# Performance work log

Measured on AMD Instinct MI355X. Metric: run time of the kernel, lower is better.

## Reference

```python
import jax, jax.numpy as jnp
import numpy as np

N = 262144   # tokens
L = 128      # ldims (per-direction LSTM feature size)
H = 128      # hidden_units
H2 = 128     # hidden2_units
R = 64       # number of relation labels


def setup_inputs() -> dict:
    key = jax.random.key(0)
    ks = jax.random.split(key, 12)
    glorot = lambda k, shape: jax.random.uniform(
        k, shape, jnp.float32, -1.0, 1.0) * np.sqrt(6.0 / (shape[0] + shape[1]))
    return {
        "fwd": jax.random.normal(ks[0], (N, L), jnp.float32),
        "bwd": jax.random.normal(ks[1], (N, L), jnp.float32),
        "gold_heads": jax.random.randint(ks[2], (N - 1,), 0, N),
        "gold_rels": jax.random.randint(ks[3], (N - 1,), 0, R),
        "WFOH": glorot(ks[4], (2 * L, H)),
        "WFOM": glorot(ks[5], (2 * L, H)),
        "rhidBias": glorot(ks[6], (1, H)),
        "rcatBias": glorot(ks[7], (1, 2 * H)),
        "rhid2Layer": glorot(ks[8], (2 * H, H2)),
        "rhid2Bias": glorot(ks[9], (1, H2)),
        "routLayer": glorot(ks[10], (H2, R)),
        "routBias": glorot(ks[11], (1, R)),
    }


def reference(fwd, bwd, gold_heads, gold_rels, WFOH, WFOM, rhidBias,
              rcatBias, rhid2Layer, rhid2Bias, routLayer, routBias):
    E = gold_heads.shape[0]
    mods = jnp.arange(E) + 1                       # modifiers are tokens 1..N-1
    # per-edge concat(head fwd-state, modifier bwd-state): (E, 2L)
    cat = jnp.concatenate([fwd[gold_heads], bwd[mods]], axis=-1)
    headfov = cat @ WFOH                           # (E, H)
    modfov = cat @ WFOM                            # (E, H)
    # hidden2_units > 0 branch of __evaluateLabel
    h = jnp.tanh(jnp.concatenate([headfov, modfov], axis=-1) + rcatBias)  # (E, 2H)
    h2 = jnp.tanh(h @ rhid2Layer + rhid2Bias)      # (E, H2)
    scores = h2 @ routLayer + routBias             # (E, R)
    # hinge: best wrong label vs gold label, loss only if margin violated
    gold_s = jnp.take_along_axis(scores, gold_rels[:, None], axis=1)[:, 0]
    masked = jnp.where(jnp.arange(R)[None, :] == gold_rels[:, None], -jnp.inf, scores)
    wrong_idx = jnp.argmax(masked, axis=1)
    wrong_s = jnp.take_along_axis(scores, wrong_idx[:, None], axis=1)[:, 0]
    lerrs = jnp.where(gold_s < wrong_s + 1.0, wrong_s - gold_s, 0.0)  # (E,)
    return lerrs
```

## Files before the change

kernel.cpp:

```cpp
#include <hip/hip_runtime.h>
#include <hip/hip_bf16.h>

typedef __bf16 bf16x8 __attribute__((ext_vector_type(8)));
typedef float  f32x4  __attribute__((ext_vector_type(4)));

#define MFMA16 __builtin_amdgcn_mfma_f32_16x16x32_bf16

__device__ __forceinline__ float fast_tanh(float x) {
    float e = __builtin_amdgcn_exp2f(x * 2.8853900817779268f);
    return 1.0f - 2.0f * __builtin_amdgcn_rcpf(e + 1.0f);
}

__device__ __forceinline__ int kinv(int ke) {
    return (ke & ~31) | ((ke & 1) << 4) | ((ke >> 1) & 15);
}

__device__ __forceinline__ bf16x8 cvt2(const float4 a, const float4 b) {
    bf16x8 t;
    t[0] = (__bf16)a.x; t[1] = (__bf16)a.y; t[2] = (__bf16)a.z; t[3] = (__bf16)a.w;
    t[4] = (__bf16)b.x; t[5] = (__bf16)b.y; t[6] = (__bf16)b.z; t[7] = (__bf16)b.w;
    return t;
}

__global__ __launch_bounds__(256) void preconv_kernel(
    const float* __restrict__ WFOH, const float* __restrict__ WFOM,
    const float* __restrict__ rhid2Layer, const float* __restrict__ routLayer,
    char* __restrict__ ws)
{
    const int f = blockIdx.x * 256 + threadIdx.x;
    bf16x8 v;
    char* dst;
    if (f < 8192) {
        const int lane = f & 63, t = f >> 6;
        const int nbl = t & 1, kk = (t >> 1) & 7, w = t >> 4;
        const int g = lane >> 4, c = lane & 15;
        const int nb = 32 * w + 16 * nbl;
        const float* Wsrc = (nb < 128) ? WFOH : WFOM;
        const int col = (nb + c) & 127;
        #pragma unroll
        for (int j = 0; j < 8; ++j) v[j] = (__bf16)Wsrc[(32 * kk + 8 * g + j) * 128 + col];
        dst = ws + (size_t)f * 16;
    } else if (f < 12288) {
        const int f2 = f - 8192;
        const int lane = f2 & 63, t = f2 >> 6;
        const int nbl = t & 1, kk = (t >> 1) & 7, q4 = t >> 4;
        const int g = lane >> 4, c = lane & 15;
        const int n2 = 32 * q4 + 16 * nbl + c;
        #pragma unroll
        for (int j = 0; j < 8; ++j) v[j] = (__bf16)rhid2Layer[kinv(32 * kk + 8 * g + j) * 128 + n2];
        dst = ws + 131072 + (size_t)f2 * 16;
    } else if (f < 13312) {
        const int f3 = f - 12288;
        const int lane = f3 & 63, t = f3 >> 6;
        const int kk = t & 3, nb = t >> 2;
        const int g = lane >> 4, c = lane & 15;
        const int n3 = 16 * nb + c;
        #pragma unroll
        for (int j = 0; j < 8; ++j) v[j] = (__bf16)routLayer[(32 * kk + 8 * g + j) * 64 + n3];
        dst = ws + 196608 + (size_t)f3 * 16;
    } else {
        return;
    }
    *(bf16x8*)dst = v;
}

template<bool PRE>
__device__ __forceinline__ bf16x8 wfrag1(const char* ws, const float* WFOH, const float* WFOM,
                                         int w, int kk, int nbl, int lane) {
    if constexpr (PRE) {
        return *(const bf16x8*)(ws + (size_t)w * 16384 + kk * 2048 + nbl * 1024 + lane * 16);
    } else {
        const int g = lane >> 4, c = lane & 15;
        const int nb = 32 * w + 16 * nbl;
        const float* Wsrc = (nb < 128) ? WFOH : WFOM;
        const int col = (nb + c) & 127;
        bf16x8 v;
        #pragma unroll
        for (int j = 0; j < 8; ++j) v[j] = (__bf16)Wsrc[(32 * kk + 8 * g + j) * 128 + col];
        return v;
    }
}
template<bool PRE>
__device__ __forceinline__ bf16x8 wfrag2(const char* ws, const float* rhid2Layer,
                                         int q4, int kk, int nbl, int lane) {
    if constexpr (PRE) {
        return *(const bf16x8*)(ws + 131072 + (size_t)q4 * 16384 + kk * 2048 + nbl * 1024 + lane * 16);
    } else {
        const int g = lane >> 4, c = lane & 15;
        const int n2 = 32 * q4 + 16 * nbl + c;
        bf16x8 v;
        #pragma unroll
        for (int j = 0; j < 8; ++j) v[j] = (__bf16)rhid2Layer[kinv(32 * kk + 8 * g + j) * 128 + n2];
        return v;
    }
}
template<bool PRE>
__device__ __forceinline__ bf16x8 wfrag3(const char* ws, const float* routLayer,
                                         int nb, int kk, int lane) {
    if constexpr (PRE) {
        return *(const bf16x8*)(ws + 196608 + (size_t)nb * 4096 + kk * 1024 + lane * 16);
    } else {
        const int g = lane >> 4, c = lane & 15;
        const int n3 = 16 * nb + c;
        bf16x8 v;
        #pragma unroll
        for (int j = 0; j < 8; ++j) v[j] = (__bf16)routLayer[(32 * kk + 8 * g + j) * 64 + n3];
        return v;
    }
}

template<bool PRE>
__global__ __launch_bounds__(512, 2) void rel_kernel(
    const float* __restrict__ fwd, const float* __restrict__ bwd,
    const int* __restrict__ gold_heads, const int* __restrict__ gold_rels,
    const float* __restrict__ WFOH, const float* __restrict__ WFOM,
    const float* __restrict__ rcatBias, const float* __restrict__ rhid2Layer,
    const float* __restrict__ rhid2Bias, const float* __restrict__ routLayer,
    const float* __restrict__ routBias, const char* __restrict__ wstab,
    int* __restrict__ fixcnt, int* __restrict__ fixlist, int fixcap,
    float* __restrict__ out, int E, int NT)
{
    __shared__ __align__(16) char smem[65536];

    const int tid   = threadIdx.x;
    const int w     = tid >> 6;
    const int lane  = tid & 63;
    const int row16 = lane & 15;
    const int g     = lane >> 4;

    const int r_s = tid >> 3;
    const int q_s = tid & 7;

    const float rcb0 = rcatBias[32 * w + row16];
    const float rcb1 = rcatBias[32 * w + 16 + row16];
    const float r2b  = rhid2Bias[16 * w + row16];
    float rob[4];
    #pragma unroll
    for (int nb = 0; nb < 4; ++nb) rob[nb] = routBias[16 * nb + row16];

    bf16x8 pfb[4];
    {
        const int e = blockIdx.x * 64 + r_s;
        int nh0 = 0;
        if (q_s < 4 && e < E) nh0 = gold_heads[e];
        if (e < E) {
            const float* src = (q_s < 4) ? (fwd + (size_t)nh0 * 128 + 32 * q_s)
                                         : (bwd + (size_t)(e + 1) * 128 + 32 * (q_s - 4));
            const float4* p4 = (const float4*)src;
            #pragma unroll
            for (int i = 0; i < 4; ++i) pfb[i] = cvt2(p4[2 * i], p4[2 * i + 1]);
        } else {
            #pragma unroll
            for (int i = 0; i < 4; ++i) pfb[i] = cvt2(make_float4(0.f,0.f,0.f,0.f), make_float4(0.f,0.f,0.f,0.f));
        }
    }

    int pp = 0;
    for (int tile = blockIdx.x; tile < NT; tile += gridDim.x, pp ^= 1) {
        char* const sh_cat = smem + (pp ? 32768 : 0);
        char* const sh_h   = smem + (pp ? 0 : 32768);
        char* const sh_h2  = sh_cat;

        const int e0 = tile * 64;
        const int tnext = tile + gridDim.x;
        const bool hn = tnext < NT;

        int zoff = 0;
        asm volatile("" : "+v"(zoff));
        const char*  wsL  = wstab + zoff;
        const float* W1aL = WFOH + zoff;
        const float* W1bL = WFOM + zoff;
        const float* W2L  = rhid2Layer + zoff;
        const float* W3L  = routLayer + zoff;

        int nh = 0; bool gv = false;
        if (hn) {
            const int en = tnext * 64 + r_s;
            gv = en < E;
            if (q_s < 4 && gv) nh = gold_heads[en];
        }

        #pragma unroll
        for (int i = 0; i < 4; ++i)
            *(bf16x8*)(sh_cat + r_s * 512 + 16 * ((4 * q_s + i + r_s) & 31)) = pfb[i];

        int gr[4] = {0, 0, 0, 0};
        if (w < 4) {
            #pragma unroll
            for (int i = 0; i < 4; ++i) {
                const int e = e0 + 16 * w + 4 * g + i;
                if (e < E) gr[i] = gold_rels[e];
            }
        }
        __syncthreads();

        float4 pfA[8];
        if (hn && gv) {
            const float4* p4 = (const float4*)((q_s < 4)
                                 ? (fwd + (size_t)nh * 128 + 32 * q_s)
                                 : (bwd + (size_t)(tnext * 64 + r_s + 1) * 128 + 32 * (q_s - 4)));
            #pragma unroll
            for (int i = 0; i < 8; ++i) pfA[i] = p4[i];
        } else {
            #pragma unroll
            for (int i = 0; i < 8; ++i) pfA[i] = make_float4(0.f, 0.f, 0.f, 0.f);
        }

        f32x4 acc1[4][2];
        #pragma unroll
        for (int i = 0; i < 4; ++i) {
            acc1[i][0] = (f32x4){0.f, 0.f, 0.f, 0.f};
            acc1[i][1] = (f32x4){0.f, 0.f, 0.f, 0.f};
        }
        __builtin_amdgcn_s_setprio(1);
        #pragma unroll
        for (int kk = 0; kk < 8; ++kk) {
            const bf16x8 b0 = wfrag1<PRE>(wsL, W1aL, W1bL, w, kk, 0, lane);
            const bf16x8 b1 = wfrag1<PRE>(wsL, W1aL, W1bL, w, kk, 1, lane);
            #pragma unroll
            for (int mb = 0; mb < 4; ++mb) {
                const int R = 16 * mb + row16;
                const bf16x8 a = *(const bf16x8*)(sh_cat + R * 512 + 16 * ((4 * kk + g + R) & 31));
                acc1[mb][0] = MFMA16(a, b0, acc1[mb][0], 0, 0, 0);
                acc1[mb][1] = MFMA16(a, b1, acc1[mb][1], 0, 0, 0);
            }
        }
        __builtin_amdgcn_s_setprio(0);
        #pragma unroll
        for (int mb = 0; mb < 4; ++mb) {
            #pragma unroll
            for (int r = 0; r < 4; ++r) {
                const int row = 16 * mb + 4 * g + r;
                const __bf16 p0 = (__bf16)fast_tanh(acc1[mb][0][r] + rcb0);
                const __bf16 p1 = (__bf16)fast_tanh(acc1[mb][1][r] + rcb1);
                const unsigned uval = (unsigned)__builtin_bit_cast(unsigned short, p0)
                                    | ((unsigned)__builtin_bit_cast(unsigned short, p1) << 16);
                const int u = 4 * w + (row16 >> 2);
                *(unsigned*)(sh_h + row * 512 + 16 * ((u + row) & 31) + 4 * (row16 & 3)) = uval;
            }
        }
        __syncthreads();

        f32x4 acc2[4];
        #pragma unroll
        for (int i = 0; i < 4; ++i) acc2[i] = (f32x4){0.f, 0.f, 0.f, 0.f};
        __builtin_amdgcn_s_setprio(1);
        #pragma unroll
        for (int kk = 0; kk < 8; ++kk) {
            const bf16x8 b2 = wfrag2<PRE>(wsL, W2L, w >> 1, kk, w & 1, lane);
            #pragma unroll
            for (int mb = 0; mb < 4; ++mb) {
                const int R = 16 * mb + row16;
                const bf16x8 a = *(const bf16x8*)(sh_h + R * 512 + 16 * ((4 * kk + g + R) & 31));
                acc2[mb] = MFMA16(a, b2, acc2[mb], 0, 0, 0);
            }
        }
        __builtin_amdgcn_s_setprio(0);
        #pragma unroll
        for (int mb = 0; mb < 4; ++mb) {
            #pragma unroll
            for (int r = 0; r < 4; ++r) {
                const int row = 16 * mb + 4 * g + r;
                const __bf16 p = (__bf16)fast_tanh(acc2[mb][r] + r2b);
                const int u2 = 2 * w + (row16 >> 3);
                *(unsigned short*)(sh_h2 + row * 256 + 16 * ((u2 + row) & 15) + 2 * (row16 & 7))
                    = __builtin_bit_cast(unsigned short, p);
            }
        }
        #pragma unroll
        for (int i = 0; i < 4; ++i) pfb[i] = cvt2(pfA[2 * i], pfA[2 * i + 1]);
        __syncthreads();

        if (w < 4) {
            bf16x8 a3[4];
            #pragma unroll
            for (int kk = 0; kk < 4; ++kk) {
                const int R3 = 16 * w + row16;
                a3[kk] = *(const bf16x8*)(sh_h2 + R3 * 256 + 16 * ((4 * kk + g + R3) & 15));
            }
            f32x4 acc3[4];
            __builtin_amdgcn_s_setprio(1);
            #pragma unroll
            for (int nb = 0; nb < 4; ++nb) {
                acc3[nb] = (f32x4){0.f, 0.f, 0.f, 0.f};
                #pragma unroll
                for (int kk = 0; kk < 4; ++kk) {
                    const bf16x8 b = wfrag3<PRE>(wsL, W3L, nb, kk, lane);
                    acc3[nb] = MFMA16(a3[kk], b, acc3[nb], 0, 0, 0);
                }
            }
            __builtin_amdgcn_s_setprio(0);
            #pragma unroll
            for (int i = 0; i < 4; ++i) {
                const int gold = gr[i];
                float gs = -3.0e38f, ws_ = -3.0e38f;
                #pragma unroll
                for (int nb = 0; nb < 4; ++nb) {
                    const float v = acc3[nb][i] + rob[nb];
                    const int lab = 16 * nb + row16;
                    if (lab == gold) gs = v; else ws_ = fmaxf(ws_, v);
                }
                gs = fmaxf(gs, __shfl_xor(gs, 1)); ws_ = fmaxf(ws_, __shfl_xor(ws_, 1));
                gs = fmaxf(gs, __shfl_xor(gs, 2)); ws_ = fmaxf(ws_, __shfl_xor(ws_, 2));
                gs = fmaxf(gs, __shfl_xor(gs, 4)); ws_ = fmaxf(ws_, __shfl_xor(ws_, 4));
                gs = fmaxf(gs, __shfl_xor(gs, 8)); ws_ = fmaxf(ws_, __shfl_xor(ws_, 8));
                const int e = e0 + 16 * w + 4 * g + i;
                if (row16 == 0 && e < E) {
                    out[e] = (gs < ws_ + 1.0f) ? (ws_ - gs) : 0.0f;
                    if (fabsf((gs - ws_) - 1.0f) < 0.125f && fixcap > 0) {
                        const int idx = atomicAdd(fixcnt, 1);
                        if (idx < fixcap) fixlist[idx] = e;
                    }
                }
            }
        }
    }
}

__global__ __launch_bounds__(256) void fixup_kernel(
    const float* __restrict__ fwd, const float* __restrict__ bwd,
    const int* __restrict__ gold_heads, const int* __restrict__ gold_rels,
    const float* __restrict__ WFOH, const float* __restrict__ WFOM,
    const float* __restrict__ rcatBias, const float* __restrict__ rhid2Layer,
    const float* __restrict__ rhid2Bias, const float* __restrict__ routLayer,
    const float* __restrict__ routBias,
    const int* __restrict__ fixcnt, const int* __restrict__ fixlist, int fixcap,
    float* __restrict__ out)
{
    __shared__ float fx_cat[256];
    __shared__ float fx_h[256];
    __shared__ float fx_h2[128];
    __shared__ float fx_p[256];
    int n = *fixcnt;
    if (n > fixcap) n = fixcap;
    const int tid = threadIdx.x;
    for (int i = blockIdx.x; i < n; i += gridDim.x) {
        const int e = fixlist[i];
        {
            const int head = gold_heads[e];
            fx_cat[tid] = (tid < 128) ? fwd[(size_t)head * 128 + tid]
                                      : bwd[(size_t)(e + 1) * 128 + (tid - 128)];
        }
        __syncthreads();
        {
            const float* base = (tid < 128) ? WFOH : WFOM;
            const int col = tid & 127;
            float s = 0.f;
            #pragma unroll 8
            for (int k = 0; k < 256; ++k) s += fx_cat[k] * base[k * 128 + col];
            fx_h[tid] = tanhf(s + rcatBias[tid]);
        }
        __syncthreads();
        {
            const int d = tid & 127, hh = tid >> 7;
            float s = 0.f;
            #pragma unroll 8
            for (int k = 128 * hh; k < 128 * hh + 128; ++k) s += fx_h[k] * rhid2Layer[k * 128 + d];
            fx_p[hh * 128 + d] = s;
        }
        __syncthreads();
        if (tid < 128) fx_h2[tid] = tanhf(fx_p[tid] + fx_p[128 + tid] + rhid2Bias[tid]);
        __syncthreads();
        {
            const int d = tid & 63, qq = tid >> 6;
            float s = 0.f;
            #pragma unroll 8
            for (int k = 32 * qq; k < 32 * qq + 32; ++k) s += fx_h2[k] * routLayer[k * 64 + d];
            fx_p[qq * 64 + d] = s;
        }
        __syncthreads();
        if (tid < 64) {
            const float v = fx_p[tid] + fx_p[64 + tid] + fx_p[128 + tid] + fx_p[192 + tid] + routBias[tid];
            const int gold = gold_rels[e];
            float gs = (tid == gold) ? v : -3.0e38f;
            float wv = (tid == gold) ? -3.0e38f : v;
            #pragma unroll
            for (int o = 1; o < 64; o <<= 1) {
                gs = fmaxf(gs, __shfl_xor(gs, o));
                wv = fmaxf(wv, __shfl_xor(wv, o));
            }
            if (tid == 0) out[e] = (gs < wv + 1.0f) ? (wv - gs) : 0.0f;
        }
        __syncthreads();
    }
}

extern "C" void kernel_launch(void* const* d_in, const int* in_sizes, int n_in,
                              void* d_out, int out_size, void* d_ws, size_t ws_size,
                              hipStream_t stream) {
    const float* fwd        = (const float*)d_in[0];
    const float* bwd        = (const float*)d_in[1];
    const int*   gold_heads = (const int*)d_in[2];
    const int*   gold_rels  = (const int*)d_in[3];
    const float* WFOH       = (const float*)d_in[4];
    const float* WFOM       = (const float*)d_in[5];
    const float* rcatBias   = (const float*)d_in[7];
    const float* rhid2      = (const float*)d_in[8];
    const float* rhid2Bias  = (const float*)d_in[9];
    const float* rout       = (const float*)d_in[10];
    const float* routBias   = (const float*)d_in[11];
    float* out = (float*)d_out;

    const int E = in_sizes[2];
    if (E <= 0) return;
    const int NT = (E + 63) / 64;
    const int grid = NT < 512 ? NT : 512;

    const size_t TAB = 212992;
    const int FIXCAP = 8192;
    const size_t FIX_BYTES = 4 + 4 * (size_t)FIXCAP;

    const bool pre = ws_size >= TAB + FIX_BYTES;
    int* fixcnt = nullptr;
    int* fixlist = nullptr;
    int fixcap = 0;
    if (pre) {
        fixcnt = (int*)((char*)d_ws + TAB);
        fixlist = fixcnt + 1;
        fixcap = FIXCAP;
    } else if (ws_size >= FIX_BYTES) {
        fixcnt = (int*)d_ws;
        fixlist = fixcnt + 1;
        fixcap = FIXCAP;
    }
    if (fixcap) hipMemsetAsync(fixcnt, 0, 4, stream);

    if (pre) {
        hipLaunchKernelGGL(preconv_kernel, dim3(52), dim3(256), 0, stream,
                           WFOH, WFOM, rhid2, rout, (char*)d_ws);
        hipLaunchKernelGGL((rel_kernel<true>), dim3(grid), dim3(512), 0, stream,
                           fwd, bwd, gold_heads, gold_rels, WFOH, WFOM, rcatBias,
                           rhid2, rhid2Bias, rout, routBias, (const char*)d_ws,
                           fixcnt, fixlist, fixcap, out, E, NT);
    } else {
        hipLaunchKernelGGL((rel_kernel<false>), dim3(grid), dim3(512), 0, stream,
                           fwd, bwd, gold_heads, gold_rels, WFOH, WFOM, rcatBias,
                           rhid2, rhid2Bias, rout, routBias, (const char*)nullptr,
                           fixcnt, fixlist, fixcap, out, E, NT);
    }
    if (fixcap) {
        hipLaunchKernelGGL(fixup_kernel, dim3(120), dim3(256), 0, stream,
                           fwd, bwd, gold_heads, gold_rels, WFOH, WFOM, rcatBias,
                           rhid2, rhid2Bias, rout, routBias,
                           fixcnt, fixlist, fixcap, out);
    }
}
```

Before: 176.9 us.

## Shrink row tile to 32 with 4-wave blocks and wider per-wave N tiles

Halves the edge tile to 32 rows and the block to 256 threads (4 waves), so each wave now computes 4 column blocks in layer 1 and 2 in layer 2. The ping-pong shared-memory buffers become fixed separate cat/h/h2 regions (40 KB instead of 64 KB). The weight pre-layout changes to match the new column-block indexing, the next-tile gather is split into two halves around the layer-2 MMA, and the grid grows to 1024 blocks. The aim is more resident blocks per CU and more reuse of each B fragment per wave, at the cost of more accumulator registers and fewer rows per weight load.

```diff
diff --git a/kernel.cpp b/kernel.cpp
--- a/kernel.cpp
+++ b/kernel.cpp
@@ -32,11 +32,10 @@
     char* dst;
     if (f < 8192) {
         const int lane = f & 63, t = f >> 6;
-        const int nbl = t & 1, kk = (t >> 1) & 7, w = t >> 4;
-        const int g = lane >> 4, c = lane & 15;
-        const int nb = 32 * w + 16 * nbl;
-        const float* Wsrc = (nb < 128) ? WFOH : WFOM;
-        const int col = (nb + c) & 127;
+        const int kk = t & 7, cb = t >> 3;
+        const int g = lane >> 4, c = lane & 15;
+        const float* Wsrc = (cb < 8) ? WFOH : WFOM;
+        const int col = (16 * cb + c) & 127;
         #pragma unroll
         for (int j = 0; j < 8; ++j) v[j] = (__bf16)Wsrc[(32 * kk + 8 * g + j) * 128 + col];
         dst = ws + (size_t)f * 16;
@@ -66,14 +65,13 @@
 
 template<bool PRE>
 __device__ __forceinline__ bf16x8 wfrag1(const char* ws, const float* WFOH, const float* WFOM,
-                                         int w, int kk, int nbl, int lane) {
+                                         int cb, int kk, int lane) {
     if constexpr (PRE) {
-        return *(const bf16x8*)(ws + (size_t)w * 16384 + kk * 2048 + nbl * 1024 + lane * 16);
+        return *(const bf16x8*)(ws + (size_t)cb * 8192 + kk * 1024 + lane * 16);
     } else {
         const int g = lane >> 4, c = lane & 15;
-        const int nb = 32 * w + 16 * nbl;
-        const float* Wsrc = (nb < 128) ? WFOH : WFOM;
-        const int col = (nb + c) & 127;
+        const float* Wsrc = (cb < 8) ? WFOH : WFOM;
+        const int col = (16 * cb + c) & 127;
         bf16x8 v;
         #pragma unroll
         for (int j = 0; j < 8; ++j) v[j] = (__bf16)Wsrc[(32 * kk + 8 * g + j) * 128 + col];
@@ -110,7 +108,7 @@
 }
 
 template<bool PRE>
-__global__ __launch_bounds__(512, 2) void rel_kernel(
+__global__ __launch_bounds__(256, 4) void rel_kernel(
     const float* __restrict__ fwd, const float* __restrict__ bwd,
     const int* __restrict__ gold_heads, const int* __restrict__ gold_rels,
     const float* __restrict__ WFOH, const float* __restrict__ WFOM,
@@ -120,7 +118,10 @@
     int* __restrict__ fixcnt, int* __restrict__ fixlist, int fixcap,
     float* __restrict__ out, int E, int NT)
 {
-    __shared__ __align__(16) char smem[65536];
+    __shared__ __align__(16) char smem[40960];
+    char* const sh_cat = smem;
+    char* const sh_h   = smem + 16384;
+    char* const sh_h2  = smem + 32768;
 
     const int tid   = threadIdx.x;
     const int w     = tid >> 6;
@@ -131,16 +132,17 @@
     const int r_s = tid >> 3;
     const int q_s = tid & 7;
 
-    const float rcb0 = rcatBias[32 * w + row16];
-    const float rcb1 = rcatBias[32 * w + 16 + row16];
-    const float r2b  = rhid2Bias[16 * w + row16];
-    float rob[4];
+    float rcb[4], r2b[2], rob[4];
+    #pragma unroll
+    for (int nbl = 0; nbl < 4; ++nbl) rcb[nbl] = rcatBias[64 * w + 16 * nbl + row16];
+    #pragma unroll
+    for (int nbl = 0; nbl < 2; ++nbl) r2b[nbl] = rhid2Bias[32 * w + 16 * nbl + row16];
     #pragma unroll
     for (int nb = 0; nb < 4; ++nb) rob[nb] = routBias[16 * nb + row16];
 
     bf16x8 pfb[4];
     {
-        const int e = blockIdx.x * 64 + r_s;
+        const int e = blockIdx.x * 32 + r_s;
         int nh0 = 0;
         if (q_s < 4 && e < E) nh0 = gold_heads[e];
         if (e < E) {
@@ -155,13 +157,8 @@
         }
     }
 
-    int pp = 0;
-    for (int tile = blockIdx.x; tile < NT; tile += gridDim.x, pp ^= 1) {
-        char* const sh_cat = smem + (pp ? 32768 : 0);
-        char* const sh_h   = smem + (pp ? 0 : 32768);
-        char* const sh_h2  = sh_cat;
-
-        const int e0 = tile * 64;
+    for (int tile = blockIdx.x; tile < NT; tile += gridDim.x) {
+        const int e0 = tile * 32;
         const int tnext = tile + gridDim.x;
         const bool hn = tnext < NT;
 
@@ -175,7 +172,7 @@
 
         int nh = 0; bool gv = false;
         if (hn) {
-            const int en = tnext * 64 + r_s;
+            const int en = tnext * 32 + r_s;
             gv = en < E;
             if (q_s < 4 && gv) nh = gold_heads[en];
         }
@@ -185,7 +182,7 @@
             *(bf16x8*)(sh_cat + r_s * 512 + 16 * ((4 * q_s + i + r_s) & 31)) = pfb[i];
 
         int gr[4] = {0, 0, 0, 0};
-        if (w < 4) {
+        if (w < 2) {
             #pragma unroll
             for (int i = 0; i < 4; ++i) {
                 const int e = e0 + 16 * w + 4 * g + i;
@@ -194,90 +191,117 @@
         }
         __syncthreads();
 
-        float4 pfA[8];
+        const float* gsrc = nullptr;
+        if (hn) {
+            gsrc = (q_s < 4) ? (fwd + (size_t)nh * 128 + 32 * q_s)
+                             : (bwd + (size_t)(tnext * 32 + r_s + 1) * 128 + 32 * (q_s - 4));
+        }
+        float4 pfA[4];
         if (hn && gv) {
-            const float4* p4 = (const float4*)((q_s < 4)
-                                 ? (fwd + (size_t)nh * 128 + 32 * q_s)
-                                 : (bwd + (size_t)(tnext * 64 + r_s + 1) * 128 + 32 * (q_s - 4)));
-            #pragma unroll
-            for (int i = 0; i < 8; ++i) pfA[i] = p4[i];
+            const float4* p4 = (const float4*)gsrc;
+            #pragma unroll
+            for (int i = 0; i < 4; ++i) pfA[i] = p4[i];
         } else {
             #pragma unroll
-            for (int i = 0; i < 8; ++i) pfA[i] = make_float4(0.f, 0.f, 0.f, 0.f);
-        }
-
-        f32x4 acc1[4][2];
-        #pragma unroll
-        for (int i = 0; i < 4; ++i) {
-            acc1[i][0] = (f32x4){0.f, 0.f, 0.f, 0.f};
-            acc1[i][1] = (f32x4){0.f, 0.f, 0.f, 0.f};
-        }
+            for (int i = 0; i < 4; ++i) pfA[i] = make_float4(0.f, 0.f, 0.f, 0.f);
+        }
+
+        f32x4 acc1[2][4];
+        #pragma unroll
+        for (int mb = 0; mb < 2; ++mb)
+            #pragma unroll
+            for (int nbl = 0; nbl < 4; ++nbl) acc1[mb][nbl] = (f32x4){0.f, 0.f, 0.f, 0.f};
         __builtin_amdgcn_s_setprio(1);
         #pragma unroll
         for (int kk = 0; kk < 8; ++kk) {
-            const bf16x8 b0 = wfrag1<PRE>(wsL, W1aL, W1bL, w, kk, 0, lane);
-            const bf16x8 b1 = wfrag1<PRE>(wsL, W1aL, W1bL, w, kk, 1, lane);
-            #pragma unroll
-            for (int mb = 0; mb < 4; ++mb) {
+            bf16x8 b[4];
+            #pragma unroll
+            for (int nbl = 0; nbl < 4; ++nbl)
+                b[nbl] = wfrag1<PRE>(wsL, W1aL, W1bL, 4 * w + nbl, kk, lane);
+            #pragma unroll
+            for (int mb = 0; mb < 2; ++mb) {
                 const int R = 16 * mb + row16;
                 const bf16x8 a = *(const bf16x8*)(sh_cat + R * 512 + 16 * ((4 * kk + g + R) & 31));
-                acc1[mb][0] = MFMA16(a, b0, acc1[mb][0], 0, 0, 0);
-                acc1[mb][1] = MFMA16(a, b1, acc1[mb][1], 0, 0, 0);
+                #pragma unroll
+                for (int nbl = 0; nbl < 4; ++nbl)
+                    acc1[mb][nbl] = MFMA16(a, b[nbl], acc1[mb][nbl], 0, 0, 0);
             }
         }
         __builtin_amdgcn_s_setprio(0);
         #pragma unroll
-        for (int mb = 0; mb < 4; ++mb) {
-            #pragma unroll
-            for (int r = 0; r < 4; ++r) {
-                const int row = 16 * mb + 4 * g + r;
-                const __bf16 p0 = (__bf16)fast_tanh(acc1[mb][0][r] + rcb0);
-                const __bf16 p1 = (__bf16)fast_tanh(acc1[mb][1][r] + rcb1);
-                const unsigned uval = (unsigned)__builtin_bit_cast(unsigned short, p0)
-                                    | ((unsigned)__builtin_bit_cast(unsigned short, p1) << 16);
-                const int u = 4 * w + (row16 >> 2);
-                *(unsigned*)(sh_h + row * 512 + 16 * ((u + row) & 31) + 4 * (row16 & 3)) = uval;
-            }
-        }
-        __syncthreads();
-
-        f32x4 acc2[4];
-        #pragma unroll
-        for (int i = 0; i < 4; ++i) acc2[i] = (f32x4){0.f, 0.f, 0.f, 0.f};
+        for (int mb = 0; mb < 2; ++mb) {
+            #pragma unroll
+            for (int p = 0; p < 2; ++p) {
+                #pragma unroll
+                for (int r = 0; r < 4; ++r) {
+                    const int row = 16 * mb + 4 * g + r;
+                    const __bf16 p0 = (__bf16)fast_tanh(acc1[mb][2 * p][r] + rcb[2 * p]);
+                    const __bf16 p1 = (__bf16)fast_tanh(acc1[mb][2 * p + 1][r] + rcb[2 * p + 1]);
+                    const unsigned uval = (unsigned)__builtin_bit_cast(unsigned short, p0)
+                                        | ((unsigned)__builtin_bit_cast(unsigned short, p1) << 16);
+                    const int u = 8 * w + 4 * p + (row16 >> 2);
+                    *(unsigned*)(sh_h + row * 512 + 16 * ((u + row) & 31) + 4 * (row16 & 3)) = uval;
+                }
+            }
+        }
+        __syncthreads();
+
+        pfb[0] = cvt2(pfA[0], pfA[1]);
+        pfb[1] = cvt2(pfA[2], pfA[3]);
+        float4 pfB[4];
+        if (hn && gv) {
+            const float4* p4 = (const float4*)gsrc;
+            #pragma unroll
+            for (int i = 0; i < 4; ++i) pfB[i] = p4[4 + i];
+        } else {
+            #pragma unroll
+            for (int i = 0; i < 4; ++i) pfB[i] = make_float4(0.f, 0.f, 0.f, 0.f);
+        }
+
+        f32x4 acc2[2][2];
+        #pragma unroll
+        for (int mb = 0; mb < 2; ++mb) {
+            acc2[mb][0] = (f32x4){0.f, 0.f, 0.f, 0.f};
+            acc2[mb][1] = (f32x4){0.f, 0.f, 0.f, 0.f};
+        }
         __builtin_amdgcn_s_setprio(1);
         #pragma unroll
         for (int kk = 0; kk < 8; ++kk) {
-            const bf16x8 b2 = wfrag2<PRE>(wsL, W2L, w >> 1, kk, w & 1, lane);
-            #pragma unroll
-            for (int mb = 0; mb < 4; ++mb) {
+            const bf16x8 b0 = wfrag2<PRE>(wsL, W2L, w, kk, 0, lane);
+            const bf16x8 b1 = wfrag2<PRE>(wsL, W2L, w, kk, 1, lane);
+            #pragma unroll
+            for (int mb = 0; mb < 2; ++mb) {
                 const int R = 16 * mb + row16;
                 const bf16x8 a = *(const bf16x8*)(sh_h + R * 512 + 16 * ((4 * kk + g + R) & 31));
-                acc2[mb] = MFMA16(a, b2, acc2[mb], 0, 0, 0);
+                acc2[mb][0] = MFMA16(a, b0, acc2[mb][0], 0, 0, 0);
+                acc2[mb][1] = MFMA16(a, b1, acc2[mb][1], 0, 0, 0);
             }
         }
         __builtin_amdgcn_s_setprio(0);
         #pragma unroll
-        for (int mb = 0; mb < 4; ++mb) {
-            #pragma unroll
-            for (int r = 0; r < 4; ++r) {
-                const int row = 16 * mb + 4 * g + r;
-                const __bf16 p = (__bf16)fast_tanh(acc2[mb][r] + r2b);
-                const int u2 = 2 * w + (row16 >> 3);
-                *(unsigned short*)(sh_h2 + row * 256 + 16 * ((u2 + row) & 15) + 2 * (row16 & 7))
-                    = __builtin_bit_cast(unsigned short, p);
-            }
-        }
-        #pragma unroll
-        for (int i = 0; i < 4; ++i) pfb[i] = cvt2(pfA[2 * i], pfA[2 * i + 1]);
-        __syncthreads();
-
-        if (w < 4) {
+        for (int mb = 0; mb < 2; ++mb) {
+            #pragma unroll
+            for (int nbl = 0; nbl < 2; ++nbl) {
+                #pragma unroll
+                for (int r = 0; r < 4; ++r) {
+                    const int row = 16 * mb + 4 * g + r;
+                    const __bf16 p = (__bf16)fast_tanh(acc2[mb][nbl][r] + r2b[nbl]);
+                    const int u2 = 4 * w + 2 * nbl + (row16 >> 3);
+                    *(unsigned short*)(sh_h2 + row * 256 + 16 * ((u2 + row) & 15) + 2 * (row16 & 7))
+                        = __builtin_bit_cast(unsigned short, p);
+                }
+            }
+        }
+        pfb[2] = cvt2(pfB[0], pfB[1]);
+        pfb[3] = cvt2(pfB[2], pfB[3]);
+        __syncthreads();
+
+        if (w < 2) {
+            const int R3 = 16 * w + row16;
             bf16x8 a3[4];
             #pragma unroll
-            for (int kk = 0; kk < 4; ++kk) {
-                const int R3 = 16 * w + row16;
+            for (int kk = 0; kk < 4; ++kk)
                 a3[kk] = *(const bf16x8*)(sh_h2 + R3 * 256 + 16 * ((4 * kk + g + R3) & 15));
-            }
             f32x4 acc3[4];
             __builtin_amdgcn_s_setprio(1);
             #pragma unroll
@@ -403,8 +427,8 @@
 
     const int E = in_sizes[2];
     if (E <= 0) return;
-    const int NT = (E + 63) / 64;
-    const int grid = NT < 512 ? NT : 512;
+    const int NT = (E + 31) / 32;
+    const int grid = NT < 1024 ? NT : 1024;
 
     const size_t TAB = 212992;
     const int FIXCAP = 8192;
@@ -428,12 +452,12 @@
     if (pre) {
         hipLaunchKernelGGL(preconv_kernel, dim3(52), dim3(256), 0, stream,
                            WFOH, WFOM, rhid2, rout, (char*)d_ws);
-        hipLaunchKernelGGL((rel_kernel<true>), dim3(grid), dim3(512), 0, stream,
+        hipLaunchKernelGGL((rel_kernel<true>), dim3(grid), dim3(256), 0, stream,
                            fwd, bwd, gold_heads, gold_rels, WFOH, WFOM, rcatBias,
                            rhid2, rhid2Bias, rout, routBias, (const char*)d_ws,
                            fixcnt, fixlist, fixcap, out, E, NT);
     } else {
-        hipLaunchKernelGGL((rel_kernel<false>), dim3(grid), dim3(512), 0, stream,
+        hipLaunchKernelGGL((rel_kernel<false>), dim3(grid), dim3(256), 0, stream,
                            fwd, bwd, gold_heads, gold_rels, WFOH, WFOM, rcatBias,
                            rhid2, rhid2Bias, rout, routBias, (const char*)nullptr,
                            fixcnt, fixlist, fixcap, out, E, NT);
```

Measured after the change: 235.2 us. 1.33x slower.

## Make each wave own a 16-edge tile end-to-end with no block barriers

Applied to the files above, without the earlier changes.

Restructures the fused MLP kernel so each wavefront independently processes a 16-row tile through all three layers, using a private LDS slice instead of block-wide shared tiles and __syncthreads. Biases are folded into accumulator init, and the weight tables and routLayer are permuted so layer outputs feed the next MFMA directly. This removes block barriers and the cross-wave split of N dimensions. In exchange each wave now streams all the weights per 16 rows, which adds weight loads from cache, and the cross-tile gather prefetch is dropped.

```diff
diff --git a/kernel.cpp b/kernel.cpp
--- a/kernel.cpp
+++ b/kernel.cpp
@@ -32,11 +32,10 @@
     char* dst;
     if (f < 8192) {
         const int lane = f & 63, t = f >> 6;
-        const int nbl = t & 1, kk = (t >> 1) & 7, w = t >> 4;
-        const int g = lane >> 4, c = lane & 15;
-        const int nb = 32 * w + 16 * nbl;
-        const float* Wsrc = (nb < 128) ? WFOH : WFOM;
-        const int col = (nb + c) & 127;
+        const int kk = t & 7, cb = t >> 3;
+        const int g = lane >> 4, c = lane & 15;
+        const float* Wsrc = (cb < 8) ? WFOH : WFOM;
+        const int col = (16 * cb + c) & 127;
         #pragma unroll
         for (int j = 0; j < 8; ++j) v[j] = (__bf16)Wsrc[(32 * kk + 8 * g + j) * 128 + col];
         dst = ws + (size_t)f * 16;
@@ -56,7 +55,7 @@
         const int g = lane >> 4, c = lane & 15;
         const int n3 = 16 * nb + c;
         #pragma unroll
-        for (int j = 0; j < 8; ++j) v[j] = (__bf16)routLayer[(32 * kk + 8 * g + j) * 64 + n3];
+        for (int j = 0; j < 8; ++j) v[j] = (__bf16)routLayer[kinv(32 * kk + 8 * g + j) * 64 + n3];
         dst = ws + 196608 + (size_t)f3 * 16;
     } else {
         return;
@@ -66,14 +65,13 @@
 
 template<bool PRE>
 __device__ __forceinline__ bf16x8 wfrag1(const char* ws, const float* WFOH, const float* WFOM,
-                                         int w, int kk, int nbl, int lane) {
+                                         int cb, int kk, int lane) {
     if constexpr (PRE) {
-        return *(const bf16x8*)(ws + (size_t)w * 16384 + kk * 2048 + nbl * 1024 + lane * 16);
+        return *(const bf16x8*)(ws + (size_t)cb * 8192 + kk * 1024 + lane * 16);
     } else {
         const int g = lane >> 4, c = lane & 15;
-        const int nb = 32 * w + 16 * nbl;
-        const float* Wsrc = (nb < 128) ? WFOH : WFOM;
-        const int col = (nb + c) & 127;
+        const float* Wsrc = (cb < 8) ? WFOH : WFOM;
+        const int col = (16 * cb + c) & 127;
         bf16x8 v;
         #pragma unroll
         for (int j = 0; j < 8; ++j) v[j] = (__bf16)Wsrc[(32 * kk + 8 * g + j) * 128 + col];
@@ -104,7 +102,7 @@
         const int n3 = 16 * nb + c;
         bf16x8 v;
         #pragma unroll
-        for (int j = 0; j < 8; ++j) v[j] = (__bf16)routLayer[(32 * kk + 8 * g + j) * 64 + n3];
+        for (int j = 0; j < 8; ++j) v[j] = (__bf16)routLayer[kinv(32 * kk + 8 * g + j) * 64 + n3];
         return v;
     }
 }
@@ -118,52 +116,18 @@
     const float* __restrict__ rhid2Bias, const float* __restrict__ routLayer,
     const float* __restrict__ routBias, const char* __restrict__ wstab,
     int* __restrict__ fixcnt, int* __restrict__ fixlist, int fixcap,
-    float* __restrict__ out, int E, int NT)
+    float* __restrict__ out, int E, int NT16)
 {
     __shared__ __align__(16) char smem[65536];
-
     const int tid   = threadIdx.x;
     const int w     = tid >> 6;
     const int lane  = tid & 63;
     const int row16 = lane & 15;
     const int g     = lane >> 4;
-
-    const int r_s = tid >> 3;
-    const int q_s = tid & 7;
-
-    const float rcb0 = rcatBias[32 * w + row16];
-    const float rcb1 = rcatBias[32 * w + 16 + row16];
-    const float r2b  = rhid2Bias[16 * w + row16];
-    float rob[4];
-    #pragma unroll
-    for (int nb = 0; nb < 4; ++nb) rob[nb] = routBias[16 * nb + row16];
-
-    bf16x8 pfb[4];
-    {
-        const int e = blockIdx.x * 64 + r_s;
-        int nh0 = 0;
-        if (q_s < 4 && e < E) nh0 = gold_heads[e];
-        if (e < E) {
-            const float* src = (q_s < 4) ? (fwd + (size_t)nh0 * 128 + 32 * q_s)
-                                         : (bwd + (size_t)(e + 1) * 128 + 32 * (q_s - 4));
-            const float4* p4 = (const float4*)src;
-            #pragma unroll
-            for (int i = 0; i < 4; ++i) pfb[i] = cvt2(p4[2 * i], p4[2 * i + 1]);
-        } else {
-            #pragma unroll
-            for (int i = 0; i < 4; ++i) pfb[i] = cvt2(make_float4(0.f,0.f,0.f,0.f), make_float4(0.f,0.f,0.f,0.f));
-        }
-    }
-
-    int pp = 0;
-    for (int tile = blockIdx.x; tile < NT; tile += gridDim.x, pp ^= 1) {
-        char* const sh_cat = smem + (pp ? 32768 : 0);
-        char* const sh_h   = smem + (pp ? 0 : 32768);
-        char* const sh_h2  = sh_cat;
-
-        const int e0 = tile * 64;
-        const int tnext = tile + gridDim.x;
-        const bool hn = tnext < NT;
+    char* const myh = smem + w * 8192;
+
+    for (int tile = blockIdx.x * 8 + w; tile < NT16; tile += gridDim.x * 8) {
+        const int e0 = tile * 16;
 
         int zoff = 0;
         asm volatile("" : "+v"(zoff));
@@ -172,145 +136,136 @@
         const float* W1bL = WFOM + zoff;
         const float* W2L  = rhid2Layer + zoff;
         const float* W3L  = routLayer + zoff;
-
-        int nh = 0; bool gv = false;
-        if (hn) {
-            const int en = tnext * 64 + r_s;
-            gv = en < E;
-            if (q_s < 4 && gv) nh = gold_heads[en];
-        }
-
-        #pragma unroll
-        for (int i = 0; i < 4; ++i)
-            *(bf16x8*)(sh_cat + r_s * 512 + 16 * ((4 * q_s + i + r_s) & 31)) = pfb[i];
-
-        int gr[4] = {0, 0, 0, 0};
-        if (w < 4) {
-            #pragma unroll
-            for (int i = 0; i < 4; ++i) {
-                const int e = e0 + 16 * w + 4 * g + i;
-                if (e < E) gr[i] = gold_rels[e];
-            }
-        }
-        __syncthreads();
-
-        float4 pfA[8];
-        if (hn && gv) {
-            const float4* p4 = (const float4*)((q_s < 4)
-                                 ? (fwd + (size_t)nh * 128 + 32 * q_s)
-                                 : (bwd + (size_t)(tnext * 64 + r_s + 1) * 128 + 32 * (q_s - 4)));
-            #pragma unroll
-            for (int i = 0; i < 8; ++i) pfA[i] = p4[i];
-        } else {
-            #pragma unroll
-            for (int i = 0; i < 8; ++i) pfA[i] = make_float4(0.f, 0.f, 0.f, 0.f);
-        }
-
-        f32x4 acc1[4][2];
-        #pragma unroll
-        for (int i = 0; i < 4; ++i) {
-            acc1[i][0] = (f32x4){0.f, 0.f, 0.f, 0.f};
-            acc1[i][1] = (f32x4){0.f, 0.f, 0.f, 0.f};
+        const float* rcL  = rcatBias + zoff;
+        const float* r2L  = rhid2Bias + zoff;
+        const float* roL  = routBias + zoff;
+
+        const int er = e0 + row16;
+        const bool ev = er < E;
+        const int head = ev ? gold_heads[er] : 0;
+        const float* frow = fwd + (size_t)head * 128;
+        const float* brow = bwd + (ev ? (size_t)(er + 1) * 128 : (size_t)0);
+        bf16x8 a[8];
+        #pragma unroll
+        for (int kk = 0; kk < 4; ++kk) {
+            const float4* p = (const float4*)(frow + 32 * kk + 8 * g);
+            a[kk] = cvt2(p[0], p[1]);
+        }
+        #pragma unroll
+        for (int kk = 0; kk < 4; ++kk) {
+            const float4* p = (const float4*)(brow + 32 * kk + 8 * g);
+            a[4 + kk] = cvt2(p[0], p[1]);
+        }
+
+        #pragma unroll
+        for (int half = 0; half < 2; ++half) {
+            f32x4 acc[8];
+            #pragma unroll
+            for (int j = 0; j < 8; ++j) {
+                const float b = rcL[16 * (8 * half + j) + row16];
+                acc[j] = (f32x4){b, b, b, b};
+            }
+            __builtin_amdgcn_s_setprio(1);
+            #pragma unroll
+            for (int kk = 0; kk < 8; ++kk) {
+                #pragma unroll
+                for (int j = 0; j < 8; ++j) {
+                    const bf16x8 b = wfrag1<PRE>(wsL, W1aL, W1bL, 8 * half + j, kk, lane);
+                    acc[j] = MFMA16(a[kk], b, acc[j], 0, 0, 0);
+                }
+            }
+            __builtin_amdgcn_s_setprio(0);
+            #pragma unroll
+            for (int q = 0; q < 4; ++q) {
+                const int qq = 4 * half + q;
+                #pragma unroll
+                for (int r = 0; r < 4; ++r) {
+                    const int row = 4 * g + r;
+                    const __bf16 p0 = (__bf16)fast_tanh(acc[2 * q][r]);
+                    const __bf16 p1 = (__bf16)fast_tanh(acc[2 * q + 1][r]);
+                    const unsigned uval = (unsigned)__builtin_bit_cast(unsigned short, p0)
+                                        | ((unsigned)__builtin_bit_cast(unsigned short, p1) << 16);
+                    const int u = 4 * qq + (row16 >> 2);
+                    *(unsigned*)(myh + row * 512 + 16 * ((u + row) & 31) + 4 * (row16 & 3)) = uval;
+                }
+            }
+        }
+
+        #pragma unroll
+        for (int kk = 0; kk < 8; ++kk)
+            a[kk] = *(const bf16x8*)(myh + row16 * 512 + 16 * ((4 * kk + g + row16) & 31));
+
+        f32x4 acc2[8];
+        #pragma unroll
+        for (int j = 0; j < 8; ++j) {
+            const float b = r2L[16 * j + row16];
+            acc2[j] = (f32x4){b, b, b, b};
         }
         __builtin_amdgcn_s_setprio(1);
         #pragma unroll
         for (int kk = 0; kk < 8; ++kk) {
-            const bf16x8 b0 = wfrag1<PRE>(wsL, W1aL, W1bL, w, kk, 0, lane);
-            const bf16x8 b1 = wfrag1<PRE>(wsL, W1aL, W1bL, w, kk, 1, lane);
-            #pragma unroll
-            for (int mb = 0; mb < 4; ++mb) {
-                const int R = 16 * mb + row16;
-                const bf16x8 a = *(const bf16x8*)(sh_cat + R * 512 + 16 * ((4 * kk + g + R) & 31));
-                acc1[mb][0] = MFMA16(a, b0, acc1[mb][0], 0, 0, 0);
-                acc1[mb][1] = MFMA16(a, b1, acc1[mb][1], 0, 0, 0);
+            #pragma unroll
+            for (int j = 0; j < 8; ++j) {
+                const bf16x8 b = wfrag2<PRE>(wsL, W2L, j >> 1, kk, j & 1, lane);
+                acc2[j] = MFMA16(a[kk], b, acc2[j], 0, 0, 0);
             }
         }
         __builtin_amdgcn_s_setprio(0);
         #pragma unroll
-        for (int mb = 0; mb < 4; ++mb) {
+        for (int q = 0; q < 4; ++q) {
             #pragma unroll
             for (int r = 0; r < 4; ++r) {
-                const int row = 16 * mb + 4 * g + r;
-                const __bf16 p0 = (__bf16)fast_tanh(acc1[mb][0][r] + rcb0);
-                const __bf16 p1 = (__bf16)fast_tanh(acc1[mb][1][r] + rcb1);
+                const int row = 4 * g + r;
+                const __bf16 p0 = (__bf16)fast_tanh(acc2[2 * q][r]);
+                const __bf16 p1 = (__bf16)fast_tanh(acc2[2 * q + 1][r]);
                 const unsigned uval = (unsigned)__builtin_bit_cast(unsigned short, p0)
                                     | ((unsigned)__builtin_bit_cast(unsigned short, p1) << 16);
-                const int u = 4 * w + (row16 >> 2);
-                *(unsigned*)(sh_h + row * 512 + 16 * ((u + row) & 31) + 4 * (row16 & 3)) = uval;
-            }
-        }
-        __syncthreads();
-
-        f32x4 acc2[4];
-        #pragma unroll
-        for (int i = 0; i < 4; ++i) acc2[i] = (f32x4){0.f, 0.f, 0.f, 0.f};
+                const int u2 = 4 * q + (row16 >> 2);
+                *(unsigned*)(myh + row * 256 + 16 * ((u2 + row) & 15) + 4 * (row16 & 3)) = uval;
+            }
+        }
+
+        bf16x8 a3[4];
+        #pragma unroll
+        for (int kk = 0; kk < 4; ++kk)
+            a3[kk] = *(const bf16x8*)(myh + row16 * 256 + 16 * ((4 * kk + g + row16) & 15));
+
+        f32x4 acc3[4];
+        #pragma unroll
+        for (int j = 0; j < 4; ++j) {
+            const float b = roL[16 * j + row16];
+            acc3[j] = (f32x4){b, b, b, b};
+        }
         __builtin_amdgcn_s_setprio(1);
         #pragma unroll
-        for (int kk = 0; kk < 8; ++kk) {
-            const bf16x8 b2 = wfrag2<PRE>(wsL, W2L, w >> 1, kk, w & 1, lane);
-            #pragma unroll
-            for (int mb = 0; mb < 4; ++mb) {
-                const int R = 16 * mb + row16;
-                const bf16x8 a = *(const bf16x8*)(sh_h + R * 512 + 16 * ((4 * kk + g + R) & 31));
-                acc2[mb] = MFMA16(a, b2, acc2[mb], 0, 0, 0);
+        for (int kk = 0; kk < 4; ++kk) {
+            #pragma unroll
+            for (int j = 0; j < 4; ++j) {
+                const bf16x8 b = wfrag3<PRE>(wsL, W3L, j, kk, lane);
+                acc3[j] = MFMA16(a3[kk], b, acc3[j], 0, 0, 0);
             }
         }
         __builtin_amdgcn_s_setprio(0);
         #pragma unroll
-        for (int mb = 0; mb < 4; ++mb) {
-            #pragma unroll
-            for (int r = 0; r < 4; ++r) {
-                const int row = 16 * mb + 4 * g + r;
-                const __bf16 p = (__bf16)fast_tanh(acc2[mb][r] + r2b);
-                const int u2 = 2 * w + (row16 >> 3);
-                *(unsigned short*)(sh_h2 + row * 256 + 16 * ((u2 + row) & 15) + 2 * (row16 & 7))
-                    = __builtin_bit_cast(unsigned short, p);
-            }
-        }
-        #pragma unroll
-        for (int i = 0; i < 4; ++i) pfb[i] = cvt2(pfA[2 * i], pfA[2 * i + 1]);
-        __syncthreads();
-
-        if (w < 4) {
-            bf16x8 a3[4];
-            #pragma unroll
-            for (int kk = 0; kk < 4; ++kk) {
-                const int R3 = 16 * w + row16;
-                a3[kk] = *(const bf16x8*)(sh_h2 + R3 * 256 + 16 * ((4 * kk + g + R3) & 15));
-            }
-            f32x4 acc3[4];
-            __builtin_amdgcn_s_setprio(1);
+        for (int r = 0; r < 4; ++r) {
+            const int e = e0 + 4 * g + r;
+            const int gold = (e < E) ? gold_rels[e] : 0;
+            float gs = -3.0e38f, ws_ = -3.0e38f;
             #pragma unroll
             for (int nb = 0; nb < 4; ++nb) {
-                acc3[nb] = (f32x4){0.f, 0.f, 0.f, 0.f};
-                #pragma unroll
-                for (int kk = 0; kk < 4; ++kk) {
-                    const bf16x8 b = wfrag3<PRE>(wsL, W3L, nb, kk, lane);
-                    acc3[nb] = MFMA16(a3[kk], b, acc3[nb], 0, 0, 0);
-                }
-            }
-            __builtin_amdgcn_s_setprio(0);
-            #pragma unroll
-            for (int i = 0; i < 4; ++i) {
-                const int gold = gr[i];
-                float gs = -3.0e38f, ws_ = -3.0e38f;
-                #pragma unroll
-                for (int nb = 0; nb < 4; ++nb) {
-                    const float v = acc3[nb][i] + rob[nb];
-                    const int lab = 16 * nb + row16;
-                    if (lab == gold) gs = v; else ws_ = fmaxf(ws_, v);
-                }
-                gs = fmaxf(gs, __shfl_xor(gs, 1)); ws_ = fmaxf(ws_, __shfl_xor(ws_, 1));
-                gs = fmaxf(gs, __shfl_xor(gs, 2)); ws_ = fmaxf(ws_, __shfl_xor(ws_, 2));
-                gs = fmaxf(gs, __shfl_xor(gs, 4)); ws_ = fmaxf(ws_, __shfl_xor(ws_, 4));
-                gs = fmaxf(gs, __shfl_xor(gs, 8)); ws_ = fmaxf(ws_, __shfl_xor(ws_, 8));
-                const int e = e0 + 16 * w + 4 * g + i;
-                if (row16 == 0 && e < E) {
-                    out[e] = (gs < ws_ + 1.0f) ? (ws_ - gs) : 0.0f;
-                    if (fabsf((gs - ws_) - 1.0f) < 0.125f && fixcap > 0) {
-                        const int idx = atomicAdd(fixcnt, 1);
-                        if (idx < fixcap) fixlist[idx] = e;
-                    }
+                const float v = acc3[nb][r];
+                const int lab = 16 * nb + row16;
+                if (lab == gold) gs = v; else ws_ = fmaxf(ws_, v);
+            }
+            gs = fmaxf(gs, __shfl_xor(gs, 1)); ws_ = fmaxf(ws_, __shfl_xor(ws_, 1));
+            gs = fmaxf(gs, __shfl_xor(gs, 2)); ws_ = fmaxf(ws_, __shfl_xor(ws_, 2));
+            gs = fmaxf(gs, __shfl_xor(gs, 4)); ws_ = fmaxf(ws_, __shfl_xor(ws_, 4));
+            gs = fmaxf(gs, __shfl_xor(gs, 8)); ws_ = fmaxf(ws_, __shfl_xor(ws_, 8));
+            if (row16 == 0 && e < E) {
+                out[e] = (gs < ws_ + 1.0f) ? (ws_ - gs) : 0.0f;
+                if (fabsf((gs - ws_) - 1.0f) < 0.125f && fixcap > 0) {
+                    const int idx = atomicAdd(fixcnt, 1);
+                    if (idx < fixcap) fixlist[idx] = e;
                 }
             }
         }
@@ -403,8 +358,9 @@
 
     const int E = in_sizes[2];
     if (E <= 0) return;
-    const int NT = (E + 63) / 64;
-    const int grid = NT < 512 ? NT : 512;
+    const int NT16 = (E + 15) / 16;
+    int grid = (NT16 + 7) / 8;
+    if (grid > 2048) grid = 2048;
 
     const size_t TAB = 212992;
     const int FIXCAP = 8192;
@@ -431,12 +387,12 @@
         hipLaunchKernelGGL((rel_kernel<true>), dim3(grid), dim3(512), 0, stream,
                            fwd, bwd, gold_heads, gold_rels, WFOH, WFOM, rcatBias,
                            rhid2, rhid2Bias, rout, routBias, (const char*)d_ws,
-                           fixcnt, fixlist, fixcap, out, E, NT);
+                           fixcnt, fixlist, fixcap, out, E, NT16);
     } else {
         hipLaunchKernelGGL((rel_kernel<false>), dim3(grid), dim3(512), 0, stream,
                            fwd, bwd, gold_heads, gold_rels, WFOH, WFOM, rcatBias,
                            rhid2, rhid2Bias, rout, routBias, (const char*)nullptr,
-                           fixcnt, fixlist, fixcap, out, E, NT);
+                           fixcnt, fixlist, fixcap, out, E, NT16);
     }
     if (fixcap) {
         hipLaunchKernelGGL(fixup_kernel, dim3(120), dim3(256), 0, stream,
```

Result: slower. 224.6 us (+26.9%).
